# Kernel optimization log

Measured on AMD Instinct MI355X. Metric: run time of the kernel, lower is better.

Reference implementation:

```python
import jax, jax.numpy as jnp
import numpy as np

G = 128          # resolution
NE = 4           # n_emotions
SIGMA = 0.05     # splat kernel width
ETA = 0.01       # global write strength
ALPHA_H = 0.002
ALPHA_E = 0.001
LEAK = 5e-05
RADIUS = max(2, int(3.0 * SIGMA * G / 2.0))   # = 9
W = 2 * RADIUS + 1                            # = 19


def _laplacian(x):
    # 6-neighbor Laplacian with replicate padding; x: [..., G, G, G]
    pad = [(0, 0)] * (x.ndim - 3) + [(1, 1)] * 3
    p = jnp.pad(x, pad, mode='edge')
    c = p[..., 1:-1, 1:-1, 1:-1]
    return (p[..., :-2, 1:-1, 1:-1] + p[..., 2:, 1:-1, 1:-1]
            + p[..., 1:-1, :-2, 1:-1] + p[..., 1:-1, 2:, 1:-1]
            + p[..., 1:-1, 1:-1, :-2] + p[..., 1:-1, 1:-1, 2:]
            - 6.0 * c)


def _splat(H, E, positions, intensities, emotions):
    # Gaussian splat scatter-add into H [G,G,G] and E [NE,G,G,G].
    gp = (positions + 1.0) * 0.5 * (G - 1)                       # [N,3] grid coords
    c = jnp.clip(jnp.floor(gp).astype(jnp.int32), 0, G - 1)      # center cell
    offs = jnp.arange(-RADIUS, RADIUS + 1, dtype=jnp.int32)
    coords = c[:, :, None] + offs[None, None, :]                 # [N,3,W]
    valid = (coords >= 0) & (coords < G)
    cc = jnp.clip(coords, 0, G - 1)
    sig = SIGMA * G / 2.0
    d = coords.astype(gp.dtype) - gp[:, :, None]                 # [N,3,W]
    k1 = jnp.where(valid, jnp.exp(-(d * d) / (2.0 * sig * sig)), 0.0)
    kx, ky, kz = k1[:, 0], k1[:, 1], k1[:, 2]                    # [N,W] each (separable)
    omega = intensities * ETA                                    # [N]
    vals = (omega[:, None, None, None] * kx[:, :, None, None]
            * ky[:, None, :, None] * kz[:, None, None, :])       # [N,W,W,W]
    flat = ((cc[:, 0][:, :, None, None] * G + cc[:, 1][:, None, :, None]) * G
            + cc[:, 2][:, None, None, :]).reshape(-1)            # [N*W^3]
    H_new = H.reshape(-1).at[flat].add(vals.reshape(-1)).reshape(G, G, G)
    E_ch = []
    for e in range(NE):
        ve = (vals * emotions[:, e][:, None, None, None]).reshape(-1)
        E_ch.append(E[e].reshape(-1).at[flat].add(ve).reshape(G, G, G))
    return H_new, jnp.stack(E_ch)


def _step(H, E):
    H2 = jnp.maximum(H * (1.0 - LEAK) + ALPHA_H * _laplacian(H), 0.0)
    E2 = jnp.maximum(E * (1.0 - LEAK) + LEAK + ALPHA_E * _laplacian(E), 0.0)
    return H2, E2


def _sample(H, E, sp):
    # grid_sample trilinear, padding_mode='border', align_corners=True.
    # grid_sample axis convention: sp[...,0]->last axis, sp[...,1]->middle, sp[...,2]->first.
    B, T, _ = sp.shape
    t = jnp.clip((sp.reshape(-1, 3) + 1.0) * 0.5 * (G - 1), 0.0, G - 1)  # [BT,3]
    i0 = jnp.floor(t).astype(jnp.int32)
    f = t - i0
    i0 = jnp.clip(i0, 0, G - 1)
    i1 = jnp.clip(i0 + 1, 0, G - 1)
    x0, y0, z0 = i0[:, 0], i0[:, 1], i0[:, 2]
    x1, y1, z1 = i1[:, 0], i1[:, 1], i1[:, 2]
    fx, fy, fz = f[:, 0], f[:, 1], f[:, 2]

    def interp(vol):  # vol [..., G,G,G] -> [..., BT]
        out = 0.0
        for zi, wz in ((z0, 1.0 - fz), (z1, fz)):
            for yi, wy in ((y0, 1.0 - fy), (y1, fy)):
                for xi, wx in ((x0, 1.0 - fx), (x1, fx)):
                    out = out + vol[..., zi, yi, xi] * (wz * wy * wx)
        return out

    p_H = interp(H).reshape(B, T)
    p_E = interp(E).T.reshape(B, T, NE)
    return p_H, p_E


def setup_inputs() -> dict:
    key = jax.random.key(0)
    k1, k2, k3, k4 = jax.random.split(key, 4)
    N, B, T = 4096, 8, 1024
    return {
        'positions': jax.random.uniform(k1, (N, 3), jnp.float32, -0.95, 0.95),
        'intensities': jax.random.uniform(k2, (N,), jnp.float32),
        'emotions': jax.random.uniform(k3, (N, NE), jnp.float32),
        'sample_positions': jax.random.uniform(k4, (B, T, 3), jnp.float32, -1.0, 1.0),
        'H0': jnp.zeros((G, G, G), jnp.float32),
        'E0': jnp.ones((NE, G, G, G), jnp.float32),
    }


def reference(positions, intensities, emotions, sample_positions, H0, E0):
    H, E = _splat(H0, E0, positions, intensities, emotions)
    H, E = _step(H, E)
    p_H, p_E = _sample(H, E, sample_positions)
    return jnp.concatenate([p_H[..., None], p_E], axis=-1)  # [B,T,1+NE]
```

## Files before the change

kernel.cpp:

```cpp
#include <hip/hip_runtime.h>


namespace {
constexpr int   G      = 128;
constexpr int   G3     = G * G * G;
constexpr int   NE     = 4;
constexpr int   RAD    = 9;
constexpr float SIG    = 0.05f * (float)G * 0.5f;
constexpr float INV2S2 = 1.0f / (2.0f * SIG * SIG);
constexpr float ETA    = 0.01f;
constexpr float A_H    = 0.002f;
constexpr float A_E    = 0.001f;
constexpr float LEAK   = 5e-5f;

constexpr int T0 = 8, T1 = 8, T2 = 16;
constexpr int NT0 = G / T0, NT1 = G / T1, NT2 = G / T2;
constexpr int NTILES = NT0 * NT1 * NT2;
constexpr int CAP  = 112;
constexpr int CPAD = 113;
}

__device__ __forceinline__ int clampi(int v, int lo, int hi) {
    return min(max(v, lo), hi);
}

__global__ void zero_counts(int4* __restrict__ counts4) {
    counts4[threadIdx.x + blockIdx.x * blockDim.x] = make_int4(0, 0, 0, 0);
}

__global__ void __launch_bounds__(256) bin_meta_kernel(
        const float* __restrict__ pos, const float* __restrict__ inten,
        const float4* __restrict__ emo4,
        int* __restrict__ counts, int* __restrict__ lists,
        float4* __restrict__ meta, int N) {
    const int p    = blockIdx.x * 4 + (threadIdx.x >> 6);
    const int lane = threadIdx.x & 63;
    if (p >= N) return;

    const float gx = (pos[p * 3 + 0] + 1.0f) * 0.5f * (float)(G - 1);
    const float gy = (pos[p * 3 + 1] + 1.0f) * 0.5f * (float)(G - 1);
    const float gz = (pos[p * 3 + 2] + 1.0f) * 0.5f * (float)(G - 1);
    const int c0 = clampi((int)floorf(gx), 0, G - 1);
    const int c1 = clampi((int)floorf(gy), 0, G - 1);
    const int c2 = clampi((int)floorf(gz), 0, G - 1);

    if (lane == 0) {
        meta[2 * p]     = make_float4(gx, gy, gz, inten[p] * ETA);
        meta[2 * p + 1] = emo4[p];
    }

    const int l0 = max(c0 - RAD, 0) >> 3, h0 = min(c0 + RAD, G - 1) >> 3;
    const int l1 = max(c1 - RAD, 0) >> 3, h1 = min(c1 + RAD, G - 1) >> 3;
    const int l2 = max(c2 - RAD, 0) >> 4, h2 = min(c2 + RAD, G - 1) >> 4;
    const int n0 = h0 - l0, n1 = h1 - l1, n2 = h2 - l2;

    if (lane < 48) {
        const int a  = lane / 12;
        const int r  = lane - a * 12;
        const int b  = r / 3;
        const int cs = r - b * 3;
        if (a <= n0 && b <= n1 && cs <= n2) {
            const int t = ((l0 + a) * NT1 + (l1 + b)) * NT2 + (l2 + cs);
            const int slot = atomicAdd(&counts[t], 1);
            if (slot < CAP) lists[t * CAP + slot] = p;
        }
    }
}

__global__ void __launch_bounds__(256) gather_kernel(
        const float4* __restrict__ meta,
        const float* __restrict__ H0, const float* __restrict__ E0,
        const int* __restrict__ counts, const int* __restrict__ lists,
        float* __restrict__ ws) {
    const int tile = blockIdx.x;
    const int t2 = tile & 7, t1 = (tile >> 3) & 15, t0 = tile >> 7;
    const int tid = threadIdx.x;

    __shared__ __align__(16) float kxf[CAP * 8];
    __shared__ __align__(16) float emf[CAP * 4];
    __shared__ float kyf[8 * CPAD];
    __shared__ float kzf[16 * CPAD];

    const int b0 = t0 * T0, b1 = t1 * T1, b2 = t2 * T2;

    const int k  = tid & 15;
    const int j  = (tid >> 4) & 7;
    const int iA = tid >> 7;
    const int x2 = b2 + k, x1 = b1 + j;
    const int flat0 = ((b0 + iA) * G + x1) * G + x2;

    float h[4], e[NE][4];
#pragma unroll
    for (int i = 0; i < 4; ++i) {
        h[i] = H0[flat0 + i * 2 * G * G];
#pragma unroll
        for (int c = 0; c < NE; ++c)
            e[c][i] = E0[c * G3 + flat0 + i * 2 * G * G];
    }

    const int cnt    = min(counts[tile], CAP);
    const int padded = (cnt + 15) & ~15;

    if (tid < padded) {
        float4* kx4w = (float4*)kxf;
        if (tid < cnt) {
            const int p = lists[tile * CAP + tid];
            const float4 mg = meta[2 * p];
            const float4 me = meta[2 * p + 1];
            const int cx = clampi((int)floorf(mg.x), 0, G - 1);
            const int cy = clampi((int)floorf(mg.y), 0, G - 1);
            const int cz = clampi((int)floorf(mg.z), 0, G - 1);

            float4 kxa, kxb;
            {
                float* a = &kxa.x;
                float* b = &kxb.x;
#pragma unroll
                for (int ii = 0; ii < 4; ++ii) {
                    const int c0a = b0 + 2 * ii;
                    const int c0b = b0 + 1 + 2 * ii;
                    const float da = (float)c0a - mg.x;
                    const float db = (float)c0b - mg.x;
                    a[ii] = (abs(c0a - cx) <= RAD)
                          ? __expf(-da * da * INV2S2) * mg.w : 0.0f;
                    b[ii] = (abs(c0b - cx) <= RAD)
                          ? __expf(-db * db * INV2S2) * mg.w : 0.0f;
                }
            }
            kx4w[tid * 2 + 0] = kxa;
            kx4w[tid * 2 + 1] = kxb;

#pragma unroll
            for (int off = 0; off < 8; ++off) {
                const int coord = b1 + off;
                const float d = (float)coord - mg.y;
                kyf[off * CPAD + tid] = (abs(coord - cy) <= RAD)
                                      ? __expf(-d * d * INV2S2) : 0.0f;
            }
#pragma unroll
            for (int off = 0; off < 16; ++off) {
                const int coord = b2 + off;
                const float d = (float)coord - mg.z;
                kzf[off * CPAD + tid] = (abs(coord - cz) <= RAD)
                                      ? __expf(-d * d * INV2S2) : 0.0f;
            }
            ((float4*)emf)[tid] = me;
        } else {
            const float4 z4 = make_float4(0.f, 0.f, 0.f, 0.f);
            kx4w[tid * 2 + 0] = z4;
            kx4w[tid * 2 + 1] = z4;
        }
    }
    __syncthreads();

    const float4* __restrict__ kx4 = (const float4*)kxf;
    const float4* __restrict__ em4 = (const float4*)emf;
    const float*  __restrict__ kyp = kyf + j * CPAD;
    const float*  __restrict__ kzp = kzf + k * CPAD;

    for (int base = 0; base < padded; base += 16) {
#pragma unroll
        for (int u = 0; u < 16; ++u) {
            const int n = base + u;
            const float4 kxv = kx4[n * 2 + iA];
            const float4 emv = em4[n];
            const float kyz = kyp[n] * kzp[n];
            const float w0 = kxv.x * kyz, w1 = kxv.y * kyz;
            const float w2 = kxv.z * kyz, w3 = kxv.w * kyz;
            h[0] += w0;  h[1] += w1;  h[2] += w2;  h[3] += w3;
            e[0][0] += w0 * emv.x; e[0][1] += w1 * emv.x; e[0][2] += w2 * emv.x; e[0][3] += w3 * emv.x;
            e[1][0] += w0 * emv.y; e[1][1] += w1 * emv.y; e[1][2] += w2 * emv.y; e[1][3] += w3 * emv.y;
            e[2][0] += w0 * emv.z; e[2][1] += w1 * emv.z; e[2][2] += w2 * emv.z; e[2][3] += w3 * emv.z;
            e[3][0] += w0 * emv.w; e[3][1] += w1 * emv.w; e[3][2] += w2 * emv.w; e[3][3] += w3 * emv.w;
        }
    }

#pragma unroll
    for (int i = 0; i < 4; ++i) {
        ws[flat0 + i * 2 * G * G] = h[i];
#pragma unroll
        for (int c = 0; c < NE; ++c)
            ws[(c + 1) * G3 + flat0 + i * 2 * G * G] = e[c][i];
    }
}

__device__ __forceinline__ float stepped_at(const float* __restrict__ vol,
                                            int z, int y, int x,
                                            float addc, float alpha) {
    const int zm = max(z - 1, 0), zp = min(z + 1, G - 1);
    const int ym = max(y - 1, 0), yp = min(y + 1, G - 1);
    const int xm = max(x - 1, 0), xp = min(x + 1, G - 1);
    const float cv  = vol[(z * G + y) * G + x];
    const float lap = vol[(zm * G + y) * G + x] + vol[(zp * G + y) * G + x]
                    + vol[(z * G + ym) * G + x] + vol[(z * G + yp) * G + x]
                    + vol[(z * G + y) * G + xm] + vol[(z * G + y) * G + xp]
                    - 6.0f * cv;
    const float s = cv * (1.0f - LEAK) + addc + alpha * lap;
    return fmaxf(s, 0.0f);
}

__global__ void __launch_bounds__(256) sample_kernel(
        const float* __restrict__ sp, const float* __restrict__ ws,
        float* __restrict__ out, int n_out) {
    const int gt = blockIdx.x * blockDim.x + threadIdx.x;
    const int corner = gt & 7;
    const int o = gt >> 3;
    if (o >= n_out) return;
    const int c = o % 5;
    const int p = o / 5;

    const float t0 = fminf(fmaxf((sp[p * 3 + 0] + 1.0f) * 0.5f * (float)(G - 1), 0.0f), (float)(G - 1));
    const float t1 = fminf(fmaxf((sp[p * 3 + 1] + 1.0f) * 0.5f * (float)(G - 1), 0.0f), (float)(G - 1));
    const float t2 = fminf(fmaxf((sp[p * 3 + 2] + 1.0f) * 0.5f * (float)(G - 1), 0.0f), (float)(G - 1));

    const int a0 = (int)floorf(t0);  const float f0 = t0 - (float)a0;
    const int a1 = (int)floorf(t1);  const float f1 = t1 - (float)a1;
    const int a2 = (int)floorf(t2);  const float f2 = t2 - (float)a2;
    const int b0 = min(a0 + 1, G - 1);
    const int b1 = min(a1 + 1, G - 1);
    const int b2 = min(a2 + 1, G - 1);

    const int d0 = corner & 1, d1 = (corner >> 1) & 1, d2 = corner >> 2;
    const int   x = d0 ? b0 : a0;
    const int   y = d1 ? b1 : a1;
    const int   z = d2 ? b2 : a2;
    const float w = (d0 ? f0 : 1.0f - f0) * (d1 ? f1 : 1.0f - f1)
                  * (d2 ? f2 : 1.0f - f2);

    const float* vol  = ws + (size_t)c * G3;
    const float addc  = (c == 0) ? 0.0f : LEAK;
    const float alpha = (c == 0) ? A_H : A_E;

    float v = w * stepped_at(vol, z, y, x, addc, alpha);
    v += __shfl_xor(v, 1);
    v += __shfl_xor(v, 2);
    v += __shfl_xor(v, 4);
    if (corner == 0) out[o] = v;
}

extern "C" void kernel_launch(void* const* d_in, const int* in_sizes, int n_in,
                              void* d_out, int out_size, void* d_ws, size_t ws_size,
                              hipStream_t stream) {
    const float* positions   = (const float*)d_in[0];
    const float* intensities = (const float*)d_in[1];
    const float* emotions    = (const float*)d_in[2];
    const float* sample_pos  = (const float*)d_in[3];
    const float* H0          = (const float*)d_in[4];
    const float* E0          = (const float*)d_in[5];
    float* ws  = (float*)d_ws;
    float* out = (float*)d_out;

    const int N = in_sizes[0] / 3;

    int*    counts = (int*)(ws + 5 * (size_t)G3);
    int*    lists  = counts + NTILES;
    float4* meta   = (float4*)(lists + (size_t)NTILES * CAP);

    zero_counts<<<2, 256, 0, stream>>>((int4*)counts);

    bin_meta_kernel<<<(N + 3) / 4, 256, 0, stream>>>(
        positions, intensities, (const float4*)emotions, counts, lists, meta, N);

    gather_kernel<<<NTILES, 256, 0, stream>>>(
        meta, H0, E0, counts, lists, ws);

    const int n_thr = out_size * 8;
    sample_kernel<<<(n_thr + 255) / 256, 256, 0, stream>>>(
        sample_pos, ws, out, out_size);
}
```

Baseline: 135.3 us.

## Store per-tile splat metadata directly in bins and vectorize ky/kz LDS reads

```diff
diff --git a/kernel.cpp b/kernel.cpp
--- a/kernel.cpp
+++ b/kernel.cpp
@@ -16,8 +16,8 @@
 constexpr int T0 = 8, T1 = 8, T2 = 16;
 constexpr int NT0 = G / T0, NT1 = G / T1, NT2 = G / T2;
 constexpr int NTILES = NT0 * NT1 * NT2;
-constexpr int CAP  = 112;
-constexpr int CPAD = 113;
+constexpr int CAP = 96;
+constexpr int PAD = 100;
 }
 
 __device__ __forceinline__ int clampi(int v, int lo, int hi) {
@@ -28,11 +28,11 @@
     counts4[threadIdx.x + blockIdx.x * blockDim.x] = make_int4(0, 0, 0, 0);
 }
 
-__global__ void __launch_bounds__(256) bin_meta_kernel(
+__global__ void __launch_bounds__(256) bin_kernel(
         const float* __restrict__ pos, const float* __restrict__ inten,
         const float4* __restrict__ emo4,
-        int* __restrict__ counts, int* __restrict__ lists,
-        float4* __restrict__ meta, int N) {
+        int* __restrict__ counts,
+        float4* __restrict__ tileG, float4* __restrict__ tileEm, int N) {
     const int p    = blockIdx.x * 4 + (threadIdx.x >> 6);
     const int lane = threadIdx.x & 63;
     if (p >= N) return;
@@ -43,11 +43,6 @@
     const int c0 = clampi((int)floorf(gx), 0, G - 1);
     const int c1 = clampi((int)floorf(gy), 0, G - 1);
     const int c2 = clampi((int)floorf(gz), 0, G - 1);
-
-    if (lane == 0) {
-        meta[2 * p]     = make_float4(gx, gy, gz, inten[p] * ETA);
-        meta[2 * p + 1] = emo4[p];
-    }
 
     const int l0 = max(c0 - RAD, 0) >> 3, h0 = min(c0 + RAD, G - 1) >> 3;
     const int l1 = max(c1 - RAD, 0) >> 3, h1 = min(c1 + RAD, G - 1) >> 3;
@@ -62,24 +57,27 @@
         if (a <= n0 && b <= n1 && cs <= n2) {
             const int t = ((l0 + a) * NT1 + (l1 + b)) * NT2 + (l2 + cs);
             const int slot = atomicAdd(&counts[t], 1);
-            if (slot < CAP) lists[t * CAP + slot] = p;
+            if (slot < CAP) {
+                const size_t idx = (size_t)t * CAP + slot;
+                tileG[idx]  = make_float4(gx, gy, gz, inten[p] * ETA);
+                tileEm[idx] = emo4[p];
+            }
         }
     }
 }
 
 __global__ void __launch_bounds__(256) gather_kernel(
-        const float4* __restrict__ meta,
+        const float4* __restrict__ tileG, const float4* __restrict__ tileEm,
         const float* __restrict__ H0, const float* __restrict__ E0,
-        const int* __restrict__ counts, const int* __restrict__ lists,
-        float* __restrict__ ws) {
+        const int* __restrict__ counts, float* __restrict__ ws) {
     const int tile = blockIdx.x;
+    const int cnt  = min(counts[tile], CAP);
     const int t2 = tile & 7, t1 = (tile >> 3) & 15, t0 = tile >> 7;
     const int tid = threadIdx.x;
 
     __shared__ __align__(16) float kxf[CAP * 8];
-    __shared__ __align__(16) float emf[CAP * 4];
-    __shared__ float kyf[8 * CPAD];
-    __shared__ float kzf[16 * CPAD];
+    __shared__ __align__(16) float kyf[8 * PAD];
+    __shared__ __align__(16) float kzf[16 * PAD];
 
     const int b0 = t0 * T0, b1 = t1 * T1, b2 = t2 * T2;
 
@@ -98,15 +96,12 @@
             e[c][i] = E0[c * G3 + flat0 + i * 2 * G * G];
     }
 
-    const int cnt    = min(counts[tile], CAP);
     const int padded = (cnt + 15) & ~15;
 
     if (tid < padded) {
         float4* kx4w = (float4*)kxf;
         if (tid < cnt) {
-            const int p = lists[tile * CAP + tid];
-            const float4 mg = meta[2 * p];
-            const float4 me = meta[2 * p + 1];
+            const float4 mg = tileG[(size_t)tile * CAP + tid];
             const int cx = clampi((int)floorf(mg.x), 0, G - 1);
             const int cy = clampi((int)floorf(mg.y), 0, G - 1);
             const int cz = clampi((int)floorf(mg.z), 0, G - 1);
@@ -134,44 +129,55 @@
             for (int off = 0; off < 8; ++off) {
                 const int coord = b1 + off;
                 const float d = (float)coord - mg.y;
-                kyf[off * CPAD + tid] = (abs(coord - cy) <= RAD)
-                                      ? __expf(-d * d * INV2S2) : 0.0f;
+                kyf[off * PAD + tid] = (abs(coord - cy) <= RAD)
+                                     ? __expf(-d * d * INV2S2) : 0.0f;
             }
 #pragma unroll
             for (int off = 0; off < 16; ++off) {
                 const int coord = b2 + off;
                 const float d = (float)coord - mg.z;
-                kzf[off * CPAD + tid] = (abs(coord - cz) <= RAD)
-                                      ? __expf(-d * d * INV2S2) : 0.0f;
-            }
-            ((float4*)emf)[tid] = me;
+                kzf[off * PAD + tid] = (abs(coord - cz) <= RAD)
+                                     ? __expf(-d * d * INV2S2) : 0.0f;
+            }
         } else {
             const float4 z4 = make_float4(0.f, 0.f, 0.f, 0.f);
             kx4w[tid * 2 + 0] = z4;
             kx4w[tid * 2 + 1] = z4;
+#pragma unroll
+            for (int off = 0; off < 8; ++off)  kyf[off * PAD + tid] = 0.0f;
+#pragma unroll
+            for (int off = 0; off < 16; ++off) kzf[off * PAD + tid] = 0.0f;
         }
     }
     __syncthreads();
 
     const float4* __restrict__ kx4 = (const float4*)kxf;
-    const float4* __restrict__ em4 = (const float4*)emf;
-    const float*  __restrict__ kyp = kyf + j * CPAD;
-    const float*  __restrict__ kzp = kzf + k * CPAD;
+    const float4* __restrict__ emp = tileEm + (size_t)tile * CAP;
+    const float*  __restrict__ kyp = kyf + j * PAD;
+    const float*  __restrict__ kzp = kzf + k * PAD;
 
     for (int base = 0; base < padded; base += 16) {
 #pragma unroll
-        for (int u = 0; u < 16; ++u) {
-            const int n = base + u;
-            const float4 kxv = kx4[n * 2 + iA];
-            const float4 emv = em4[n];
-            const float kyz = kyp[n] * kzp[n];
-            const float w0 = kxv.x * kyz, w1 = kxv.y * kyz;
-            const float w2 = kxv.z * kyz, w3 = kxv.w * kyz;
-            h[0] += w0;  h[1] += w1;  h[2] += w2;  h[3] += w3;
-            e[0][0] += w0 * emv.x; e[0][1] += w1 * emv.x; e[0][2] += w2 * emv.x; e[0][3] += w3 * emv.x;
-            e[1][0] += w0 * emv.y; e[1][1] += w1 * emv.y; e[1][2] += w2 * emv.y; e[1][3] += w3 * emv.y;
-            e[2][0] += w0 * emv.z; e[2][1] += w1 * emv.z; e[2][2] += w2 * emv.z; e[2][3] += w3 * emv.z;
-            e[3][0] += w0 * emv.w; e[3][1] += w1 * emv.w; e[3][2] += w2 * emv.w; e[3][3] += w3 * emv.w;
+        for (int q = 0; q < 4; ++q) {
+            const int n4 = base + q * 4;
+            const float4 ky4 = *(const float4*)(kyp + n4);
+            const float4 kz4 = *(const float4*)(kzp + n4);
+            const float kyu[4] = {ky4.x, ky4.y, ky4.z, ky4.w};
+            const float kzu[4] = {kz4.x, kz4.y, kz4.z, kz4.w};
+#pragma unroll
+            for (int u = 0; u < 4; ++u) {
+                const int n = n4 + u;
+                const float4 kxv = kx4[n * 2 + iA];
+                const float4 emv = emp[n];
+                const float kyz = kyu[u] * kzu[u];
+                const float w0 = kxv.x * kyz, w1 = kxv.y * kyz;
+                const float w2 = kxv.z * kyz, w3 = kxv.w * kyz;
+                h[0] += w0;  h[1] += w1;  h[2] += w2;  h[3] += w3;
+                e[0][0] += w0 * emv.x; e[0][1] += w1 * emv.x; e[0][2] += w2 * emv.x; e[0][3] += w3 * emv.x;
+                e[1][0] += w0 * emv.y; e[1][1] += w1 * emv.y; e[1][2] += w2 * emv.y; e[1][3] += w3 * emv.y;
+                e[2][0] += w0 * emv.z; e[2][1] += w1 * emv.z; e[2][2] += w2 * emv.z; e[2][3] += w3 * emv.z;
+                e[3][0] += w0 * emv.w; e[3][1] += w1 * emv.w; e[3][2] += w2 * emv.w; e[3][3] += w3 * emv.w;
+            }
         }
     }
 
@@ -253,16 +259,17 @@
     const int N = in_sizes[0] / 3;
 
     int*    counts = (int*)(ws + 5 * (size_t)G3);
-    int*    lists  = counts + NTILES;
-    float4* meta   = (float4*)(lists + (size_t)NTILES * CAP);
+    float4* tileG  = (float4*)(counts + NTILES);
+    float4* tileEm = tileG + (size_t)NTILES * CAP;
 
     zero_counts<<<2, 256, 0, stream>>>((int4*)counts);
 
-    bin_meta_kernel<<<(N + 3) / 4, 256, 0, stream>>>(
-        positions, intensities, (const float4*)emotions, counts, lists, meta, N);
+    bin_kernel<<<(N + 3) / 4, 256, 0, stream>>>(
+        positions, intensities, (const float4*)emotions,
+        counts, tileG, tileEm, N);
 
     gather_kernel<<<NTILES, 256, 0, stream>>>(
-        meta, H0, E0, counts, lists, ws);
+        tileG, tileEm, H0, E0, counts, ws);
 
     const int n_thr = out_size * 8;
     sample_kernel<<<(n_thr + 255) / 256, 256, 0, stream>>>(
```

After: 142.4 us. 5.2% more time.
